# Performance work log

Hardware: AMD Instinct MI355X
Metric: run time of the kernel (lower is better)

The kernel has to match this reference:

```python
import jax, jax.numpy as jnp
from jax import lax
import numpy as np

B, L, D, HS, T, N = 1024, 96, 128, 512, 24, 128  # batch, former_seq_len, input_dim, hidden_dim, output_dim, temp_node


def setup_inputs() -> dict:
    key = jax.random.key(0)
    ks = jax.random.split(key, 14)
    s = 1.0 / np.sqrt(HS)  # init std used by the torch module
    f32 = jnp.float32
    return {
        "H": jax.random.normal(ks[0], (B, L, D), f32),
        "y_0": jax.random.normal(ks[1], (B, 1), f32),
        "embedding": jax.random.normal(ks[2], (B, 2 * HS), f32),
        "Y": jax.random.normal(ks[3], (B, T), f32),
        "Wa": jax.random.normal(ks[4], (D, T, N), f32) * s,
        "Ua": jax.random.normal(ks[5], (HS, T, N), f32) * s,
        "ba": jax.random.normal(ks[6], (T, N), f32) * s,
        "Va": jax.random.normal(ks[7], (N, T, 1), f32) * s,
        "W": jax.random.normal(ks[8], (D, T, 4 * HS), f32) * s,
        "U": jax.random.normal(ks[9], (HS, T, 4 * HS), f32) * s,
        "bias": jax.random.normal(ks[10], (T, 4 * HS), f32) * s,
        "W_y": jax.random.normal(ks[11], (1, T, 4 * HS), f32) * s,
        "fc_w": jax.random.normal(ks[12], (T, HS), f32) * s,  # output_fc[t].weight (row vec)
        "fc_b": jax.random.normal(ks[13], (T,), f32) * s,      # output_fc[t].bias
        "epoch": 3,
    }


def reference(H, y_0, embedding, Y, Wa, Ua, ba, Va, W, U, bias, W_y, fc_w, fc_b, epoch):
    scale = 1.0 / jnp.sqrt(jnp.asarray(HS, H.dtype))
    h0 = embedding[:, :HS]
    c0 = embedding[:, HS:]

    # time-major parameter stacks for lax.scan
    xs = (
        jnp.transpose(Wa, (1, 0, 2)),   # [T, D, N]
        jnp.transpose(Ua, (1, 0, 2)),   # [T, HS, N]
        ba,                              # [T, N]
        jnp.transpose(Va, (1, 0, 2)),   # [T, N, 1]
        jnp.transpose(W, (1, 0, 2)),    # [T, D, 4HS]
        jnp.transpose(U, (1, 0, 2)),    # [T, HS, 4HS]
        bias,                            # [T, 4HS]
        jnp.transpose(W_y, (1, 0, 2)),  # [T, 1, 4HS]
        fc_w,                            # [T, HS]
        fc_b,                            # [T]
    )

    def step(carry, p):
        h_l, c_l, y_prev = carry  # [B,HS], [B,HS], [B,1]
        wa, ua, ba_t, va, w, u, b, wy, fw, fb = p
        # temporal attention over the encoder history
        e = jnp.tanh(jnp.einsum('bld,dn->bln', H, wa) + (c_l @ ua)[:, None, :] + ba_t)  # [B,L,N]
        score = jnp.einsum('bln,n->bl', e, va[:, 0]) * scale                              # [B,L]
        beta = jax.nn.softmax(score, axis=1)
        h_t = jnp.einsum('bl,bld->bd', beta, H)                                           # [B,D]
        # 4-gate LSTM update with teacher-signal injection
        gates = h_t @ w + h_l @ u + b + y_prev @ wy                                       # [B,4HS]
        i = jax.nn.sigmoid(gates[:, :HS])
        f = jax.nn.sigmoid(gates[:, HS:2 * HS])
        g = jnp.tanh(gates[:, 2 * HS:3 * HS])
        o = jax.nn.sigmoid(gates[:, 3 * HS:])
        c_new = f * c_l + i * g
        h_new = o * jnp.tanh(c_new)
        y = h_new @ fw + fb                                                               # [B]
        return (h_new, c_new, y[:, None]), (y, h_new)

    _, (ys, hs) = lax.scan(step, (h0, c0, y_0), xs)
    y_out = ys.T                           # [B, T]
    hidden_seq = jnp.transpose(hs, (1, 0, 2))  # [B, T, HS]
    return y_out, hidden_seq
```

## Files before the change

kernel.cpp:

```cpp
#include <hip/hip_runtime.h>
#include <math.h>

constexpr int NB  = 1024;
constexpr int NL  = 96;
constexpr int ND  = 128;
constexpr int NHS = 512;
constexpr int NT  = 24;
constexpr int NN  = 128;
constexpr int NG4 = 4 * NHS;
constexpr int NK  = ND + NHS;
constexpr int BL  = NB * NL;

typedef __attribute__((ext_vector_type(8))) short bf16x8;
typedef __attribute__((ext_vector_type(4))) float f32x4;

static __device__ __forceinline__ unsigned short f2b(float x) {
    union { float f; unsigned u; } v; v.f = x;
    unsigned r = v.u + 0x7fffu + ((v.u >> 16) & 1u);
    return (unsigned short)(r >> 16);
}
static __device__ __forceinline__ float b2f(unsigned short s) {
    union { unsigned u; float f; } v; v.u = ((unsigned)s) << 16;
    return v.f;
}

constexpr float LOG2E  = 1.4426950408889634f;
static __device__ __forceinline__ float fast_exp(float x) {
    return __builtin_amdgcn_exp2f(x * LOG2E);
}
static __device__ __forceinline__ float fast_tanh(float x) {
    float e2 = __builtin_amdgcn_exp2f(x * (2.0f * LOG2E));
    return 1.0f - 2.0f * __builtin_amdgcn_rcpf(1.0f + e2);
}
static __device__ __forceinline__ float fast_sigmoid(float x) {
    float e = __builtin_amdgcn_exp2f(-x * LOG2E);
    return __builtin_amdgcn_rcpf(1.0f + e);
}

__global__ __launch_bounds__(256) void k_init(const float* __restrict__ emb,
                                              const float* __restrict__ y0,
                                              float* __restrict__ c,
                                              unsigned short* __restrict__ Ab0,
                                              float* __restrict__ y) {
    int idx = blockIdx.x * blockDim.x + threadIdx.x;
    if (idx < NB * NHS) {
        int b = idx / NHS, s = idx - b * NHS;
        Ab0[(size_t)b * NK + ND + s] = f2b(emb[b * 2 * NHS + s]);
        c[idx] = emb[b * 2 * NHS + NHS + s];
    }
    if (idx < NB) y[idx] = y0[idx];
}

__global__ __launch_bounds__(256) void k_prep(const float* __restrict__ H,
                                              unsigned short* __restrict__ Hbf) {
    int idx = (blockIdx.x * 256 + threadIdx.x) * 8;
    float4 a = *(const float4*)(H + idx);
    float4 b = *(const float4*)(H + idx + 4);
    bf16x8 o;
    o[0] = (short)f2b(a.x); o[1] = (short)f2b(a.y);
    o[2] = (short)f2b(a.z); o[3] = (short)f2b(a.w);
    o[4] = (short)f2b(b.x); o[5] = (short)f2b(b.y);
    o[6] = (short)f2b(b.z); o[7] = (short)f2b(b.w);
    *(bf16x8*)(Hbf + idx) = o;
}

__global__ __launch_bounds__(128) void k_prepwa(const float* __restrict__ Wa,
                                                unsigned short* __restrict__ Wab) {
    int tn = blockIdx.x;
    int t = tn / NN, n = tn - t * NN;
    int d = threadIdx.x;
    Wab[(size_t)tn * ND + d] = f2b(Wa[(size_t)d * (NT * NN) + t * NN + n]);
}

__global__ __launch_bounds__(256) void k_prepw(const float* __restrict__ W,
                                               const float* __restrict__ U,
                                               unsigned short* __restrict__ Wg) {
    __shared__ unsigned short ts[64][66];
    int nc = blockIdx.x;
    int kc = blockIdx.y;
    int t  = blockIdx.z;
    int tid = threadIdx.x;
    int rowt = tid >> 4;
    int n4   = (tid & 15) << 2;
#pragma unroll
    for (int i = 0; i < 4; ++i) {
        int kl = i * 16 + rowt;
        int k  = kc * 64 + kl;
        const float* src = (k < ND) ? (W + (size_t)k * (NT * NG4))
                                    : (U + (size_t)(k - ND) * (NT * NG4));
        float4 v = *(const float4*)&src[t * NG4 + nc * 64 + n4];
        ts[kl][n4 + 0] = f2b(v.x);
        ts[kl][n4 + 1] = f2b(v.y);
        ts[kl][n4 + 2] = f2b(v.z);
        ts[kl][n4 + 3] = f2b(v.w);
    }
    __syncthreads();
    size_t base = (((size_t)t * 10 + kc) * NG4 + nc * 64) * 64;
#pragma unroll
    for (int p = 0; p < 2; ++p) {
        int flat = p * 256 + tid;
        int nl = flat >> 3, k8 = (flat & 7) << 3;
        bf16x8 o;
#pragma unroll
        for (int j = 0; j < 8; ++j) o[j] = (short)ts[k8 + j][nl];
        *(bf16x8*)&Wg[base + (size_t)nl * 64 + k8] = o;
    }
}

__global__ __launch_bounds__(256) void k_cua0(const float* __restrict__ c,
                                              const float* __restrict__ Ua,
                                              float* __restrict__ cua_part) {
    __shared__ float cs[16][64];
    int m0 = blockIdx.x * 16, n0 = blockIdx.y;
    int tid = threadIdx.x;
#pragma unroll
    for (int i = 0; i < 4; ++i) {
        int idx = tid + i * 256;
        int row = idx >> 6, k = idx & 63;
        cs[row][k] = c[(size_t)(m0 + row) * NHS + n0 * 64 + k];
    }
    __syncthreads();
    int n = tid & 127, bg = tid >> 7;
    float a8[8] = {0, 0, 0, 0, 0, 0, 0, 0};
    for (int k = 0; k < 64; ++k) {
        float ua = Ua[(size_t)(n0 * 64 + k) * (NT * NN) + n];
#pragma unroll
        for (int i = 0; i < 8; ++i) a8[i] += cs[bg * 8 + i][k] * ua;
    }
#pragma unroll
    for (int i = 0; i < 8; ++i)
        cua_part[((size_t)(m0 + bg * 8 + i) * 8 + n0) * 128 + n] = a8[i];
}

__global__ __launch_bounds__(384, 2) void k_attn_fused(
        const unsigned short* __restrict__ Hbf,
        const unsigned short* __restrict__ Wab,
        const float* __restrict__ Va,
        const float* __restrict__ ba,
        const float* __restrict__ cua_part,
        const float* __restrict__ fcb,
        const float* __restrict__ y_part,
        float* __restrict__ y_st,
        float* __restrict__ out_y,
        unsigned short* __restrict__ Ab,
        int t) {
    __shared__ unsigned short Ws[NN][136];
    __shared__ float sc[NL];
    __shared__ float cua_s[NN];
    __shared__ float red[24][ND];
    int tid = threadIdx.x;
    int b = blockIdx.x;

    const unsigned short* src = Wab + (size_t)t * NN * ND;
    for (int f = tid; f < 2048; f += 384) {
        int n = f >> 4, d0 = (f & 15) << 3;
        *(bf16x8*)&Ws[n][d0] = *(const bf16x8*)(src + n * ND + d0);
    }
    if (tid < 128) {
        const float* cp = cua_part + (size_t)b * 8 * 128 + tid;
        float s = ba[t * NN + tid];
#pragma unroll
        for (int p = 0; p < 8; ++p) s += cp[p * 128];
        cua_s[tid] = s;
    }
    if (t > 0 && tid == 383) {
        const float* yp = y_part + (size_t)b * 8;
        float yv = fcb[t - 1];
#pragma unroll
        for (int p = 0; p < 8; ++p) yv += yp[p];
        y_st[b] = yv;
        out_y[b * NT + (t - 1)] = yv;
    }
    __syncthreads();

    int lane = tid & 63, wave = tid >> 6;
    int ln = lane & 15, kg = lane >> 4;
    const unsigned short* Hrow = Hbf + ((size_t)b * NL + wave * 16 + ln) * ND;

    f32x4 zero = {0.f, 0.f, 0.f, 0.f};
    f32x4 acc[8];
#pragma unroll
    for (int nt = 0; nt < 8; ++nt) acc[nt] = zero;
#pragma unroll
    for (int kc = 0; kc < 4; ++kc) {
        int d0 = kc * 32 + kg * 8;
        bf16x8 a = *(const bf16x8*)(Hrow + d0);
#pragma unroll
        for (int nt = 0; nt < 8; ++nt) {
            bf16x8 bb = *(const bf16x8*)&Ws[nt * 16 + ln][d0];
            acc[nt] = __builtin_amdgcn_mfma_f32_16x16x32_bf16(a, bb, acc[nt], 0, 0, 0);
        }
    }
    float va_l[8];
#pragma unroll
    for (int nt = 0; nt < 8; ++nt) va_l[nt] = Va[(nt * 16 + ln) * NT + t];
    const float scale = 0.044194173824159216f;
#pragma unroll
    for (int r = 0; r < 4; ++r) {
        float s = 0.f;
#pragma unroll
        for (int nt = 0; nt < 8; ++nt) {
            float pre = acc[nt][r] + cua_s[nt * 16 + ln];
            s += va_l[nt] * fast_tanh(pre);
        }
#pragma unroll
        for (int off = 1; off < 16; off <<= 1) s += __shfl_xor(s, off);
        if (ln == 0) sc[wave * 16 + kg * 4 + r] = s * scale;
    }
    __syncthreads();

    if (tid < 64) {
        float s0 = sc[tid];
        float s1 = (tid < 32) ? sc[64 + tid] : -1e30f;
        float m = fmaxf(s0, s1);
#pragma unroll
        for (int off = 32; off; off >>= 1) m = fmaxf(m, __shfl_xor(m, off));
        float p0 = fast_exp(s0 - m);
        float p1 = (tid < 32) ? fast_exp(s1 - m) : 0.f;
        float ssum = p0 + p1;
#pragma unroll
        for (int off = 32; off; off >>= 1) ssum += __shfl_xor(ssum, off);
        float inv = __builtin_amdgcn_rcpf(ssum);
        sc[tid] = p0 * inv;
        if (tid < 32) sc[64 + tid] = p1 * inv;
    }
    __syncthreads();

    int dc = tid & 15, lg = tid >> 4;
    int d0 = dc * 8;
    const unsigned short* Hb = Hbf + (size_t)b * NL * ND;
    float a8[8] = {0, 0, 0, 0, 0, 0, 0, 0};
#pragma unroll
    for (int i = 0; i < 4; ++i) {
        int l = lg * 4 + i;
        bf16x8 hv = *(const bf16x8*)(Hb + l * ND + d0);
        float w = sc[l];
#pragma unroll
        for (int j = 0; j < 8; ++j) a8[j] += w * b2f((unsigned short)hv[j]);
    }
#pragma unroll
    for (int j = 0; j < 8; ++j) red[lg][d0 + j] = a8[j];
    __syncthreads();
    if (tid < ND) {
        float accd = 0.f;
#pragma unroll
        for (int g = 0; g < 24; ++g) accd += red[g][tid];
        Ab[(size_t)b * NK + tid] = f2b(accd);
    }
}

__global__ __launch_bounds__(512) void k_gates_cell(
        const unsigned short* __restrict__ Ab,
        unsigned short* __restrict__ AbN,
        const unsigned short* __restrict__ Wg,
        const float* __restrict__ bias,
        const float* __restrict__ Wy,
        const float* __restrict__ fcw,
        const float* __restrict__ Ua,
        const float* __restrict__ y_st,
        float* __restrict__ c,
        float* __restrict__ out_h,
        float* __restrict__ y_part,
        float* __restrict__ cua_part,
        int t) {
    __shared__ float gs[4][32][68];
    __shared__ float cs[32][68];
    int tid = threadIdx.x;
    int lane = tid & 63, wave = tid >> 6;
    int ln = lane & 15, kg = lane >> 4;
    int m0 = blockIdx.x * 32, n0 = blockIdx.y;
    int g = wave >> 1, hf = wave & 1;
    int cb = g * NHS + n0 * 64 + hf * 32;

    const unsigned short* A0 = Ab + (size_t)(m0 + ln) * NK;
    const unsigned short* A1 = Ab + (size_t)(m0 + 16 + ln) * NK;

    f32x4 zero = {0.f, 0.f, 0.f, 0.f};
    f32x4 acc[2][2];
#pragma unroll
    for (int rt = 0; rt < 2; ++rt)
#pragma unroll
        for (int nt = 0; nt < 2; ++nt) acc[rt][nt] = zero;

    for (int kb = 0; kb < 10; ++kb) {
        const unsigned short* Wkb = Wg + ((size_t)(t * 10 + kb) * NG4) * 64;
#pragma unroll
        for (int kc = 0; kc < 2; ++kc) {
            int d0 = kc * 32 + kg * 8;
            bf16x8 a0 = *(const bf16x8*)(A0 + kb * 64 + d0);
            bf16x8 a1 = *(const bf16x8*)(A1 + kb * 64 + d0);
#pragma unroll
            for (int nt = 0; nt < 2; ++nt) {
                bf16x8 bb = *(const bf16x8*)(Wkb + (size_t)(cb + nt * 16 + ln) * 64 + d0);
                acc[0][nt] = __builtin_amdgcn_mfma_f32_16x16x32_bf16(a0, bb, acc[0][nt], 0, 0, 0);
                acc[1][nt] = __builtin_amdgcn_mfma_f32_16x16x32_bf16(a1, bb, acc[1][nt], 0, 0, 0);
            }
        }
    }
#pragma unroll
    for (int rt = 0; rt < 2; ++rt)
#pragma unroll
        for (int nt = 0; nt < 2; ++nt)
#pragma unroll
            for (int r = 0; r < 4; ++r)
                gs[g][rt * 16 + kg * 4 + r][hf * 32 + nt * 16 + ln] = acc[rt][nt][r];
    __syncthreads();

    int s_loc = tid & 63, rg = tid >> 6;
    int s_glob = n0 * 64 + s_loc;
    float bi0 = bias[t * NG4 + s_glob];
    float bi1 = bias[t * NG4 + NHS + s_glob];
    float bi2 = bias[t * NG4 + 2 * NHS + s_glob];
    float bi3 = bias[t * NG4 + 3 * NHS + s_glob];
    float wy0 = Wy[t * NG4 + s_glob];
    float wy1 = Wy[t * NG4 + NHS + s_glob];
    float wy2 = Wy[t * NG4 + 2 * NHS + s_glob];
    float wy3 = Wy[t * NG4 + 3 * NHS + s_glob];
    float fw  = fcw[t * NHS + s_glob];
    float prow[4];
#pragma unroll
    for (int i = 0; i < 4; ++i) {
        int row = rg * 4 + i;
        int b = m0 + row;
        float yp = y_st[b];
        float gi  = gs[0][row][s_loc] + bi0 + yp * wy0;
        float gf  = gs[1][row][s_loc] + bi1 + yp * wy1;
        float gg2 = gs[2][row][s_loc] + bi2 + yp * wy2;
        float go  = gs[3][row][s_loc] + bi3 + yp * wy3;
        float iv = fast_sigmoid(gi);
        float fv = fast_sigmoid(gf);
        float gv = fast_tanh(gg2);
        float ov = fast_sigmoid(go);
        float cn = fv * c[(size_t)b * NHS + s_glob] + iv * gv;
        float hn = ov * fast_tanh(cn);
        c[(size_t)b * NHS + s_glob] = cn;
        cs[row][s_loc] = cn;
        AbN[(size_t)b * NK + ND + s_glob] = f2b(hn);
        out_h[(size_t)b * (NT * NHS) + t * NHS + s_glob] = hn;
        prow[i] = hn * fw;
    }
#pragma unroll
    for (int i = 0; i < 4; ++i) {
        float v = prow[i];
#pragma unroll
        for (int off = 32; off; off >>= 1) v += __shfl_xor(v, off);
        if (lane == 0) y_part[(size_t)(m0 + rg * 4 + i) * 8 + n0] = v;
    }
    __syncthreads();

    if (t + 1 < NT) {
        int n = tid & 127, bg = tid >> 7;
        float a8[8] = {0, 0, 0, 0, 0, 0, 0, 0};
        for (int k = 0; k < 64; ++k) {
            float ua = Ua[(size_t)(n0 * 64 + k) * (NT * NN) + (t + 1) * NN + n];
#pragma unroll
            for (int i = 0; i < 8; ++i) a8[i] += cs[bg * 8 + i][k] * ua;
        }
#pragma unroll
        for (int i = 0; i < 8; ++i)
            cua_part[((size_t)(m0 + bg * 8 + i) * 8 + n0) * 128 + n] = a8[i];
    }
}

__global__ __launch_bounds__(256) void k_yfin(const float* __restrict__ y_part,
                                              const float* __restrict__ fcb,
                                              float* __restrict__ out_y) {
    int b = blockIdx.x * 256 + threadIdx.x;
    if (b < NB) {
        const float* yp = y_part + (size_t)b * 8;
        float yv = fcb[NT - 1];
#pragma unroll
        for (int p = 0; p < 8; ++p) yv += yp[p];
        out_y[b * NT + (NT - 1)] = yv;
    }
}

extern "C" void kernel_launch(void* const* d_in, const int* in_sizes, int n_in,
                              void* d_out, int out_size, void* d_ws, size_t ws_size,
                              hipStream_t stream) {
    (void)in_sizes; (void)n_in; (void)out_size; (void)ws_size;
    const float* H    = (const float*)d_in[0];
    const float* y0   = (const float*)d_in[1];
    const float* emb  = (const float*)d_in[2];
    const float* Wa   = (const float*)d_in[4];
    const float* Ua   = (const float*)d_in[5];
    const float* ba   = (const float*)d_in[6];
    const float* Va   = (const float*)d_in[7];
    const float* W    = (const float*)d_in[8];
    const float* U    = (const float*)d_in[9];
    const float* bias = (const float*)d_in[10];
    const float* Wy   = (const float*)d_in[11];
    const float* fcw  = (const float*)d_in[12];
    const float* fcb  = (const float*)d_in[13];

    float* out_y = (float*)d_out;
    float* out_h = out_y + NB * NT;

    float* ws       = (float*)d_ws;
    float* c_st     = ws;
    float* y_st     = c_st + NB * NHS;
    float* y_part   = y_st + NB;
    float* cua_part = y_part + NB * 8;
    unsigned short* Hbf = (unsigned short*)(cua_part + NB * 8 * 128);
    unsigned short* Wab = Hbf + (size_t)BL * ND;
    unsigned short* Ab0 = Wab + (size_t)NT * NN * ND;
    unsigned short* Ab1 = Ab0 + (size_t)NB * NK;
    unsigned short* Wg  = Ab1 + (size_t)NB * NK;

    hipLaunchKernelGGL(k_init, dim3((NB * NHS) / 256), dim3(256), 0, stream,
                       emb, y0, c_st, Ab0, y_st);
    hipLaunchKernelGGL(k_prep, dim3(BL * ND / (256 * 8)), dim3(256), 0, stream, H, Hbf);
    hipLaunchKernelGGL(k_prepwa, dim3(NT * NN), dim3(128), 0, stream, Wa, Wab);
    hipLaunchKernelGGL(k_prepw, dim3(32, 10, 24), dim3(256), 0, stream, W, U, Wg);
    hipLaunchKernelGGL(k_cua0, dim3(64, 8), dim3(256), 0, stream, c_st, Ua, cua_part);

    for (int t = 0; t < NT; ++t) {
        unsigned short* Ab  = (t & 1) ? Ab1 : Ab0;
        unsigned short* AbN = (t & 1) ? Ab0 : Ab1;
        hipLaunchKernelGGL(k_attn_fused, dim3(NB), dim3(384), 0, stream,
                           Hbf, Wab, Va, ba, cua_part, fcb, y_part, y_st, out_y, Ab, t);
        hipLaunchKernelGGL(k_gates_cell, dim3(32, 8), dim3(512), 0, stream,
                           Ab, AbN, Wg, bias, Wy, fcw, Ua, y_st, c_st,
                           out_h, y_part, cua_part, t);
    }
    hipLaunchKernelGGL(k_yfin, dim3(NB / 256), dim3(256), 0, stream, y_part, fcb, out_y);
}
```

Measured before the change: 1.323 ms.

## Process four batch rows per attention block and double gate-cell M tile

The attention kernel now handles four batch elements per 512-thread block. Each block loads the per-step Wa tile into shared memory once and reuses it across 24 MFMA row tiles, which cuts the redundant weight staging and the number of blocks. The gates/cell kernel uses a 64-row M tile instead of 32, so each weight fragment feeds four MFMAs, and it reuses the gate shared buffer to hold the new cell state for the next-step Ua projection. The trade-off is fewer blocks (256 and 128), which lowers parallelism on a large GPU, plus more register pressure from the larger accumulators.

Result: slower. 1.413 ms (+6.8%).

```diff
diff --git a/kernel.cpp b/kernel.cpp
--- a/kernel.cpp
+++ b/kernel.cpp
@@ -132,7 +132,7 @@
         cua_part[((size_t)(m0 + bg * 8 + i) * 8 + n0) * 128 + n] = a8[i];
 }
 
-__global__ __launch_bounds__(384, 2) void k_attn_fused(
+__global__ __launch_bounds__(512, 2) void k_attn4(
         const unsigned short* __restrict__ Hbf,
         const unsigned short* __restrict__ Wab,
         const float* __restrict__ Va,
@@ -144,26 +144,33 @@
         float* __restrict__ out_y,
         unsigned short* __restrict__ Ab,
         int t) {
-    __shared__ unsigned short Ws[NN][136];
-    __shared__ float sc[NL];
-    __shared__ float cua_s[NN];
-    __shared__ float red[24][ND];
+    __shared__ unsigned short Ws[NN * 136];
+    __shared__ float sc4[4][NL];
+    __shared__ float cua_s4[4][NN];
+    __shared__ float red[4][8][ND];
     int tid = threadIdx.x;
-    int b = blockIdx.x;
+    int lane = tid & 63, wave = tid >> 6;
+    int ln = lane & 15, kg = lane >> 4;
+    int b0 = blockIdx.x * 4;
+    f32x4 zero = {0.f, 0.f, 0.f, 0.f};
 
     const unsigned short* src = Wab + (size_t)t * NN * ND;
-    for (int f = tid; f < 2048; f += 384) {
-        int n = f >> 4, d0 = (f & 15) << 3;
-        *(bf16x8*)&Ws[n][d0] = *(const bf16x8*)(src + n * ND + d0);
-    }
-    if (tid < 128) {
-        const float* cp = cua_part + (size_t)b * 8 * 128 + tid;
-        float s = ba[t * NN + tid];
+#pragma unroll
+    for (int f = 0; f < 4; ++f) {
+        int idx = tid + f * 512;
+        int n = idx >> 4, d0 = (idx & 15) << 3;
+        *(bf16x8*)&Ws[n * 136 + d0] = *(const bf16x8*)(src + n * ND + d0);
+    }
+    {
+        int bl = tid >> 7, n = tid & 127;
+        const float* cp = cua_part + (size_t)(b0 + bl) * 8 * 128 + n;
+        float s = ba[t * NN + n];
 #pragma unroll
         for (int p = 0; p < 8; ++p) s += cp[p * 128];
-        cua_s[tid] = s;
-    }
-    if (t > 0 && tid == 383) {
+        cua_s4[bl][n] = s;
+    }
+    if (t > 0 && tid < 4) {
+        int b = b0 + tid;
         const float* yp = y_part + (size_t)b * 8;
         float yv = fcb[t - 1];
 #pragma unroll
@@ -173,79 +180,86 @@
     }
     __syncthreads();
 
-    int lane = tid & 63, wave = tid >> 6;
-    int ln = lane & 15, kg = lane >> 4;
-    const unsigned short* Hrow = Hbf + ((size_t)b * NL + wave * 16 + ln) * ND;
-
-    f32x4 zero = {0.f, 0.f, 0.f, 0.f};
-    f32x4 acc[8];
-#pragma unroll
-    for (int nt = 0; nt < 8; ++nt) acc[nt] = zero;
-#pragma unroll
-    for (int kc = 0; kc < 4; ++kc) {
-        int d0 = kc * 32 + kg * 8;
-        bf16x8 a = *(const bf16x8*)(Hrow + d0);
-#pragma unroll
-        for (int nt = 0; nt < 8; ++nt) {
-            bf16x8 bb = *(const bf16x8*)&Ws[nt * 16 + ln][d0];
-            acc[nt] = __builtin_amdgcn_mfma_f32_16x16x32_bf16(a, bb, acc[nt], 0, 0, 0);
+    {
+        const float scale_c = 0.044194173824159216f;
+        float va_l[8];
+#pragma unroll
+        for (int nt = 0; nt < 8; ++nt) va_l[nt] = Va[(nt * 16 + ln) * NT + t];
+#pragma unroll
+        for (int ti = 0; ti < 3; ++ti) {
+            int tau = wave + ti * 8;
+            int bl = tau / 6, r0 = (tau % 6) * 16;
+            const unsigned short* Hrow = Hbf + ((size_t)(b0 + bl) * NL + r0 + ln) * ND;
+            f32x4 acc[8];
+#pragma unroll
+            for (int nt = 0; nt < 8; ++nt) acc[nt] = zero;
+#pragma unroll
+            for (int kc = 0; kc < 4; ++kc) {
+                int d0 = kc * 32 + kg * 8;
+                bf16x8 a = *(const bf16x8*)(Hrow + d0);
+#pragma unroll
+                for (int nt = 0; nt < 8; ++nt) {
+                    bf16x8 bb = *(const bf16x8*)&Ws[(nt * 16 + ln) * 136 + d0];
+                    acc[nt] = __builtin_amdgcn_mfma_f32_16x16x32_bf16(a, bb, acc[nt], 0, 0, 0);
+                }
+            }
+#pragma unroll
+            for (int r = 0; r < 4; ++r) {
+                float s = 0.f;
+#pragma unroll
+                for (int nt = 0; nt < 8; ++nt) {
+                    float pre = acc[nt][r] + cua_s4[bl][nt * 16 + ln];
+                    s += va_l[nt] * fast_tanh(pre);
+                }
+#pragma unroll
+                for (int off = 1; off < 16; off <<= 1) s += __shfl_xor(s, off);
+                if (ln == 0) sc4[bl][r0 + kg * 4 + r] = s * scale_c;
+            }
         }
     }
-    float va_l[8];
-#pragma unroll
-    for (int nt = 0; nt < 8; ++nt) va_l[nt] = Va[(nt * 16 + ln) * NT + t];
-    const float scale = 0.044194173824159216f;
-#pragma unroll
-    for (int r = 0; r < 4; ++r) {
-        float s = 0.f;
-#pragma unroll
-        for (int nt = 0; nt < 8; ++nt) {
-            float pre = acc[nt][r] + cua_s[nt * 16 + ln];
-            s += va_l[nt] * fast_tanh(pre);
-        }
-#pragma unroll
-        for (int off = 1; off < 16; off <<= 1) s += __shfl_xor(s, off);
-        if (ln == 0) sc[wave * 16 + kg * 4 + r] = s * scale;
-    }
-    __syncthreads();
-
-    if (tid < 64) {
-        float s0 = sc[tid];
-        float s1 = (tid < 32) ? sc[64 + tid] : -1e30f;
+    __syncthreads();
+
+    if (wave < 4) {
+        float s0 = sc4[wave][lane];
+        float s1 = (lane < 32) ? sc4[wave][64 + lane] : -1e30f;
         float m = fmaxf(s0, s1);
 #pragma unroll
         for (int off = 32; off; off >>= 1) m = fmaxf(m, __shfl_xor(m, off));
         float p0 = fast_exp(s0 - m);
-        float p1 = (tid < 32) ? fast_exp(s1 - m) : 0.f;
+        float p1 = (lane < 32) ? fast_exp(s1 - m) : 0.f;
         float ssum = p0 + p1;
 #pragma unroll
         for (int off = 32; off; off >>= 1) ssum += __shfl_xor(ssum, off);
         float inv = __builtin_amdgcn_rcpf(ssum);
-        sc[tid] = p0 * inv;
-        if (tid < 32) sc[64 + tid] = p1 * inv;
-    }
-    __syncthreads();
-
-    int dc = tid & 15, lg = tid >> 4;
-    int d0 = dc * 8;
-    const unsigned short* Hb = Hbf + (size_t)b * NL * ND;
-    float a8[8] = {0, 0, 0, 0, 0, 0, 0, 0};
-#pragma unroll
-    for (int i = 0; i < 4; ++i) {
-        int l = lg * 4 + i;
-        bf16x8 hv = *(const bf16x8*)(Hb + l * ND + d0);
-        float w = sc[l];
-#pragma unroll
-        for (int j = 0; j < 8; ++j) a8[j] += w * b2f((unsigned short)hv[j]);
-    }
-#pragma unroll
-    for (int j = 0; j < 8; ++j) red[lg][d0 + j] = a8[j];
-    __syncthreads();
-    if (tid < ND) {
+        sc4[wave][lane] = p0 * inv;
+        if (lane < 32) sc4[wave][64 + lane] = p1 * inv;
+    }
+    __syncthreads();
+
+    {
+        int bl = tid >> 7, r7 = tid & 127;
+        int lg = r7 >> 4, dc = r7 & 15;
+        int d0 = dc * 8;
+        const unsigned short* Hb = Hbf + (size_t)(b0 + bl) * NL * ND;
+        float a8[8] = {0, 0, 0, 0, 0, 0, 0, 0};
+#pragma unroll
+        for (int i = 0; i < 12; ++i) {
+            int l = lg * 12 + i;
+            bf16x8 hv = *(const bf16x8*)(Hb + (size_t)l * ND + d0);
+            float w = sc4[bl][l];
+#pragma unroll
+            for (int j = 0; j < 8; ++j) a8[j] += w * b2f((unsigned short)hv[j]);
+        }
+#pragma unroll
+        for (int j = 0; j < 8; ++j) red[bl][lg][d0 + j] = a8[j];
+    }
+    __syncthreads();
+    {
+        int bl = tid >> 7, dd = tid & 127;
         float accd = 0.f;
 #pragma unroll
-        for (int g = 0; g < 24; ++g) accd += red[g][tid];
-        Ab[(size_t)b * NK + tid] = f2b(accd);
+        for (int g = 0; g < 8; ++g) accd += red[bl][g][dd];
+        Ab[(size_t)(b0 + bl) * NK + dd] = f2b(accd);
     }
 }
 
@@ -263,22 +277,18 @@
         float* __restrict__ y_part,
         float* __restrict__ cua_part,
         int t) {
-    __shared__ float gs[4][32][68];
-    __shared__ float cs[32][68];
+    __shared__ __align__(16) float gs[4 * 64 * 68];
     int tid = threadIdx.x;
     int lane = tid & 63, wave = tid >> 6;
     int ln = lane & 15, kg = lane >> 4;
-    int m0 = blockIdx.x * 32, n0 = blockIdx.y;
+    int m0 = blockIdx.x * 64, n0 = blockIdx.y;
     int g = wave >> 1, hf = wave & 1;
     int cb = g * NHS + n0 * 64 + hf * 32;
 
-    const unsigned short* A0 = Ab + (size_t)(m0 + ln) * NK;
-    const unsigned short* A1 = Ab + (size_t)(m0 + 16 + ln) * NK;
-
     f32x4 zero = {0.f, 0.f, 0.f, 0.f};
-    f32x4 acc[2][2];
-#pragma unroll
-    for (int rt = 0; rt < 2; ++rt)
+    f32x4 acc[4][2];
+#pragma unroll
+    for (int rt = 0; rt < 4; ++rt)
 #pragma unroll
         for (int nt = 0; nt < 2; ++nt) acc[rt][nt] = zero;
 
@@ -286,27 +296,33 @@
         const unsigned short* Wkb = Wg + ((size_t)(t * 10 + kb) * NG4) * 64;
 #pragma unroll
         for (int kc = 0; kc < 2; ++kc) {
-            int d0 = kc * 32 + kg * 8;
-            bf16x8 a0 = *(const bf16x8*)(A0 + kb * 64 + d0);
-            bf16x8 a1 = *(const bf16x8*)(A1 + kb * 64 + d0);
+            int dk = kb * 64 + kc * 32 + kg * 8;
+            bf16x8 a0 = *(const bf16x8*)(Ab + (size_t)(m0 + ln) * NK + dk);
+            bf16x8 a1 = *(const bf16x8*)(Ab + (size_t)(m0 + 16 + ln) * NK + dk);
+            bf16x8 a2 = *(const bf16x8*)(Ab + (size_t)(m0 + 32 + ln) * NK + dk);
+            bf16x8 a3 = *(const bf16x8*)(Ab + (size_t)(m0 + 48 + ln) * NK + dk);
 #pragma unroll
             for (int nt = 0; nt < 2; ++nt) {
-                bf16x8 bb = *(const bf16x8*)(Wkb + (size_t)(cb + nt * 16 + ln) * 64 + d0);
+                bf16x8 bb = *(const bf16x8*)(Wkb
+                    + (size_t)(cb + nt * 16 + ln) * 64 + kc * 32 + kg * 8);
                 acc[0][nt] = __builtin_amdgcn_mfma_f32_16x16x32_bf16(a0, bb, acc[0][nt], 0, 0, 0);
                 acc[1][nt] = __builtin_amdgcn_mfma_f32_16x16x32_bf16(a1, bb, acc[1][nt], 0, 0, 0);
+                acc[2][nt] = __builtin_amdgcn_mfma_f32_16x16x32_bf16(a2, bb, acc[2][nt], 0, 0, 0);
+                acc[3][nt] = __builtin_amdgcn_mfma_f32_16x16x32_bf16(a3, bb, acc[3][nt], 0, 0, 0);
             }
         }
     }
 #pragma unroll
-    for (int rt = 0; rt < 2; ++rt)
+    for (int rt = 0; rt < 4; ++rt)
 #pragma unroll
         for (int nt = 0; nt < 2; ++nt)
 #pragma unroll
             for (int r = 0; r < 4; ++r)
-                gs[g][rt * 16 + kg * 4 + r][hf * 32 + nt * 16 + ln] = acc[rt][nt][r];
-    __syncthreads();
-
-    int s_loc = tid & 63, rg = tid >> 6;
+                gs[(size_t)(g * 64 + rt * 16 + kg * 4 + r) * 68 + hf * 32 + nt * 16 + ln]
+                    = acc[rt][nt][r];
+    __syncthreads();
+
+    int s_loc = tid & 63;
     int s_glob = n0 * 64 + s_loc;
     float bi0 = bias[t * NG4 + s_glob];
     float bi1 = bias[t * NG4 + NHS + s_glob];
@@ -317,48 +333,51 @@
     float wy2 = Wy[t * NG4 + 2 * NHS + s_glob];
     float wy3 = Wy[t * NG4 + 3 * NHS + s_glob];
     float fw  = fcw[t * NHS + s_glob];
-    float prow[4];
-#pragma unroll
-    for (int i = 0; i < 4; ++i) {
-        int row = rg * 4 + i;
+    float prow[8];
+#pragma unroll
+    for (int i = 0; i < 8; ++i) {
+        int row = wave * 8 + i;
         int b = m0 + row;
         float yp = y_st[b];
-        float gi  = gs[0][row][s_loc] + bi0 + yp * wy0;
-        float gf  = gs[1][row][s_loc] + bi1 + yp * wy1;
-        float gg2 = gs[2][row][s_loc] + bi2 + yp * wy2;
-        float go  = gs[3][row][s_loc] + bi3 + yp * wy3;
+        float gi  = gs[(size_t)(0 * 64 + row) * 68 + s_loc] + bi0 + yp * wy0;
+        float gfv = gs[(size_t)(1 * 64 + row) * 68 + s_loc] + bi1 + yp * wy1;
+        float gg2 = gs[(size_t)(2 * 64 + row) * 68 + s_loc] + bi2 + yp * wy2;
+        float go  = gs[(size_t)(3 * 64 + row) * 68 + s_loc] + bi3 + yp * wy3;
         float iv = fast_sigmoid(gi);
-        float fv = fast_sigmoid(gf);
+        float fv = fast_sigmoid(gfv);
         float gv = fast_tanh(gg2);
         float ov = fast_sigmoid(go);
         float cn = fv * c[(size_t)b * NHS + s_glob] + iv * gv;
         float hn = ov * fast_tanh(cn);
         c[(size_t)b * NHS + s_glob] = cn;
-        cs[row][s_loc] = cn;
+        gs[(size_t)(0 * 64 + row) * 68 + s_loc] = cn;
         AbN[(size_t)b * NK + ND + s_glob] = f2b(hn);
         out_h[(size_t)b * (NT * NHS) + t * NHS + s_glob] = hn;
         prow[i] = hn * fw;
     }
 #pragma unroll
-    for (int i = 0; i < 4; ++i) {
+    for (int i = 0; i < 8; ++i) {
         float v = prow[i];
 #pragma unroll
         for (int off = 32; off; off >>= 1) v += __shfl_xor(v, off);
-        if (lane == 0) y_part[(size_t)(m0 + rg * 4 + i) * 8 + n0] = v;
+        if (lane == 0) y_part[(size_t)(m0 + wave * 8 + i) * 8 + n0] = v;
     }
     __syncthreads();
 
     if (t + 1 < NT) {
         int n = tid & 127, bg = tid >> 7;
-        float a8[8] = {0, 0, 0, 0, 0, 0, 0, 0};
+        float a16[16];
+#pragma unroll
+        for (int i = 0; i < 16; ++i) a16[i] = 0.f;
         for (int k = 0; k < 64; ++k) {
             float ua = Ua[(size_t)(n0 * 64 + k) * (NT * NN) + (t + 1) * NN + n];
 #pragma unroll
-            for (int i = 0; i < 8; ++i) a8[i] += cs[bg * 8 + i][k] * ua;
+            for (int i = 0; i < 16; ++i)
+                a16[i] += gs[(size_t)(bg * 16 + i) * 68 + k] * ua;
         }
 #pragma unroll
-        for (int i = 0; i < 8; ++i)
-            cua_part[((size_t)(m0 + bg * 8 + i) * 8 + n0) * 128 + n] = a8[i];
+        for (int i = 0; i < 16; ++i)
+            cua_part[((size_t)(m0 + bg * 16 + i) * 8 + n0) * 128 + n] = a16[i];
     }
 }
 
@@ -417,9 +436,9 @@
     for (int t = 0; t < NT; ++t) {
         unsigned short* Ab  = (t & 1) ? Ab1 : Ab0;
         unsigned short* AbN = (t & 1) ? Ab0 : Ab1;
-        hipLaunchKernelGGL(k_attn_fused, dim3(NB), dim3(384), 0, stream,
+        hipLaunchKernelGGL(k_attn4, dim3(NB / 4), dim3(512), 0, stream,
                            Hbf, Wab, Va, ba, cua_part, fcb, y_part, y_st, out_y, Ab, t);
-        hipLaunchKernelGGL(k_gates_cell, dim3(32, 8), dim3(512), 0, stream,
+        hipLaunchKernelGGL(k_gates_cell, dim3(16, 8), dim3(512), 0, stream,
                            Ab, AbN, Wg, bias, Wy, fcw, Ua, y_st, c_st,
                            out_h, y_part, cua_part, t);
     }
```
